# Optimization experiments

Measured on AMD Instinct MI355X. Metric: run time of the kernel, lower is better.

Reference implementation:

```python
import jax, jax.numpy as jnp
import numpy as np

MAX_DET = 300   # max_det in non_max_suppression
IMG = 640       # input image H=W
MH = MW = 160   # proto mask resolution
NM = 32         # mask coefficients
ALPHA = 0.6
MARGIN = 15


def setup_inputs() -> dict:
    key = jax.random.key(0)
    k1, k2, k3, k4, k5, k6 = jax.random.split(key, 6)
    na = 8400
    # realistic YOLOv8 raw head output: xywh in pixels, 1 class score in (0,1), 32 mask coeffs
    cxcy = jax.random.uniform(k1, (1, 2, na), minval=0.0, maxval=float(IMG))
    wh = jax.random.uniform(k2, (1, 2, na), minval=10.0, maxval=200.0)
    cls = jax.random.uniform(k3, (1, 1, na))
    mcoef = jax.random.normal(k4, (1, NM, na))
    prediction = jnp.concatenate([cxcy, wh, cls, mcoef], axis=1)  # [1,37,8400]
    proto = jax.random.normal(k5, (1, NM, MH, MW))
    img = jax.random.uniform(k6, (1, 3, IMG, IMG))
    return {"prediction": prediction, "proto": proto, "img": img,
            "conf_thres": jnp.float32(0.25), "iou_thres": jnp.float32(0.45)}


def _xywh2xyxy(x):
    cx, cy, w, h = x[..., 0], x[..., 1], x[..., 2], x[..., 3]
    return jnp.stack([cx - w / 2, cy - h / 2, cx + w / 2, cy + h / 2], axis=-1)


def _box_iou(b):  # b: [K,4] xyxy -> [K,K] pairwise IoU (torchvision convention)
    x1, y1, x2, y2 = b[:, 0], b[:, 1], b[:, 2], b[:, 3]
    area = (x2 - x1) * (y2 - y1)
    iw = jnp.clip(jnp.minimum(x2[:, None], x2[None, :]) - jnp.maximum(x1[:, None], x1[None, :]), 0)
    ih = jnp.clip(jnp.minimum(y2[:, None], y2[None, :]) - jnp.maximum(y1[:, None], y1[None, :]), 0)
    inter = iw * ih
    return inter / (area[:, None] + area[None, :] - inter + 1e-7)


def _nms_keep(iou, valid, iou_thres):
    # sequential greedy suppression over score-sorted boxes (padded, fixed K)
    K = iou.shape[0]
    def body(keep, i):
        suppressed = jnp.any(keep & (iou[i] > iou_thres))
        keep = keep.at[i].set(valid[i] & ~suppressed)
        return keep, None
    keep, _ = jax.lax.scan(body, jnp.zeros((K,), bool), jnp.arange(K))
    return keep


def reference(prediction, proto, img, conf_thres, iou_thres):
    # --- decode: [1,37,na] -> [na,37], xywh->xyxy (bs=1, nc=1, class offset c = 0*max_wh = 0)
    p = prediction[0].T                      # [na,37]
    boxes = _xywh2xyxy(p[:, :4])             # [na,4]
    conf = p[:, 4]                           # nc=1 -> max over classes is the class itself, j=0
    mcoef = p[:, 5:]                         # [na,32]
    valid = conf > conf_thres
    score = jnp.where(valid, conf, -1.0)
    order = jnp.argsort(-score)[:MAX_DET]    # top max_det candidates by confidence
    boxes_k, score_k, m_k = boxes[order], score[order], mcoef[order]
    valid_k = valid[order]
    # --- NMS (padded)
    keep = _nms_keep(_box_iou(boxes_k), valid_k, iou_thres)  # [K] bool
    # --- process_mask: linear combine protos, sigmoid, crop, bilinear upsample, >0.5
    masks = jax.nn.sigmoid(m_k @ proto[0].reshape(NM, -1)).reshape(MAX_DET, MH, MW)
    scale = jnp.array([MW / IMG, MH / IMG, MW / IMG, MH / IMG], dtype=boxes_k.dtype)
    db = boxes_k * scale                     # downsampled bboxes [K,4]
    r = jnp.arange(MW, dtype=masks.dtype)[None, None, :]
    c = jnp.arange(MH, dtype=masks.dtype)[None, :, None]
    crop = ((r >= db[:, 0, None, None]) & (r < db[:, 2, None, None]) &
            (c >= db[:, 1, None, None]) & (c < db[:, 3, None, None]))
    masks = masks * crop
    masks_up = jax.image.resize(masks, (MAX_DET, IMG, IMG), method='linear')  # align_corners=False bilinear
    masks_bin = (masks_up > 0.5) & keep[:, None, None]       # invalid/suppressed rows zeroed
    # --- scale_boxes: img1_shape == img0_shape -> gain=1, pad=0, just clip
    boxes_c = jnp.clip(boxes_k, 0.0, float(IMG))
    results = jnp.concatenate([boxes_c, score_k[:, None], jnp.zeros((MAX_DET, 1), boxes_c.dtype)], axis=1)
    results = results * keep[:, None].astype(results.dtype)  # [K,6] padded detections
    # --- max-area box -> crop window coords
    areas = jnp.where(keep, (boxes_c[:, 2] - boxes_c[:, 0]) * (boxes_c[:, 3] - boxes_c[:, 1]), 0.0)
    mb = jnp.where(jnp.any(keep), boxes_c[jnp.argmax(areas)], jnp.zeros(4, boxes_c.dtype))
    y1 = jnp.maximum(mb[1].astype(jnp.int32) - MARGIN, 0)
    y2 = jnp.minimum(mb[3].astype(jnp.int32) + MARGIN, IMG)
    x1 = jnp.maximum(mb[0].astype(jnp.int32) - MARGIN, 0)
    x2 = jnp.minimum(mb[2].astype(jnp.int32) + MARGIN, IMG)
    crop_coords = jnp.stack([y1, y2, x1, x2])
    # --- mask overlay blending (stack over images, sum over detections)
    stacked_mk = jnp.sum(masks_bin.astype(img.dtype), axis=0)[None]  # [1,640,640]
    pixels = jnp.count_nonzero(stacked_mk)
    blue = jnp.zeros((3, IMG, IMG), img.dtype).at[2].set(1.0)
    img_out = (1.0 - stacked_mk) * img + stacked_mk * (ALPHA * img + (1.0 - ALPHA) * blue)
    return results, keep, masks_bin, pixels, img_out, crop_coords
```

## Files before the change

kernel.cpp:

```cpp
#include <hip/hip_runtime.h>
#include <stdint.h>

#define NA 8400
#define MAXD 300
#define NMC 32
#define IMGD 640
#define MH 160
#define MW 160
#define PROTO_HW (MH*MW)
#define IMG_HW (IMGD*IMGD)

#define OFF_RESULTS 0
#define OFF_KEEP    1800
#define OFF_MASKS   2100
#define OFF_PIXELS  (2100 + 300*IMG_HW)
#define OFF_IMG     (OFF_PIXELS + 1)
#define OFF_CROP    (OFF_IMG + 3*IMG_HW)

#define WSO_MASKS160 0
#define WSO_META     (MAXD*PROTO_HW*4)
#define WSO_BOXES    (WSO_META + 64)
#define WSO_MCOEF    (WSO_BOXES + MAXD*16)
#define WSO_KEEPI    (WSO_MCOEF + MAXD*NMC*4)
#define WSO_KLIST    (WSO_KEEPI + MAXD*4)
#define WSO_EBOX     (WSO_KLIST + MAXD*4)

__global__ __launch_bounds__(1024)
void k_selnms(const float* __restrict__ pred, const float* __restrict__ conf_thres_p,
              const float* __restrict__ iou_thres_p,
              int* __restrict__ keepi, int* __restrict__ klist, int* __restrict__ meta,
              int* __restrict__ ebox, float* __restrict__ boxes_k,
              float* __restrict__ mcoef_k, float* __restrict__ out) {
    __shared__ unsigned cum[1024];
    __shared__ uint64_t kl[2048];
    __shared__ uint64_t srt[MAXD];
    __shared__ int s_cnt, s_bcut, s_nsel;
    __shared__ int sorder[MAXD];
    __shared__ int svf[MAXD];
    __shared__ float sscore[MAXD];
    __shared__ float bx[MAXD][4];
    __shared__ float sarea[MAXD];
    __shared__ uint64_t su[MAXD][5];
    __shared__ int skeep[MAXD];
    int t = threadIdx.x;
    float th = *conf_thres_p;

    cum[t] = 0;
    __syncthreads();
    for (int i = t; i < NA; i += 1024) {
        float conf = pred[4 * NA + i];
        if (conf > th) {
            int bin = (int)(conf * 1024.0f);
            bin = bin < 0 ? 0 : (bin > 1023 ? 1023 : bin);
            atomicAdd(&cum[bin], 1u);
        }
    }
    __syncthreads();
    for (int off = 1; off < 1024; off <<= 1) {
        unsigned v = cum[t] + ((t + off < 1024) ? cum[t + off] : 0u);
        __syncthreads();
        cum[t] = v;
        __syncthreads();
    }
    if (t == 0) {
        s_cnt = 0;
        int tot = (int)cum[0];
        s_nsel = tot < MAXD ? tot : MAXD;
        s_bcut = 0;
    }
    __syncthreads();
    int nsel = s_nsel;
    if (nsel > 0) {
        if (cum[t] >= (unsigned)nsel && (t == 1023 || cum[t + 1] < (unsigned)nsel))
            s_bcut = t;
    }
    __syncthreads();
    int bcut = s_bcut;
    if (nsel > 0) {
        for (int i = t; i < NA; i += 1024) {
            float conf = pred[4 * NA + i];
            if (conf > th) {
                int bin = (int)(conf * 1024.0f);
                bin = bin < 0 ? 0 : (bin > 1023 ? 1023 : bin);
                if (bin >= bcut) {
                    int p = atomicAdd(&s_cnt, 1);
                    if (p < 2048) {
                        unsigned fb = __float_as_uint(conf);
                        kl[p] = ((uint64_t)fb << 32) | (unsigned)(NA - 1 - i);
                    }
                }
            }
        }
    }
    __syncthreads();
    int cnt = s_cnt < 2048 ? s_cnt : 2048;
    for (int c = t; c < cnt; c += 1024) {
        uint64_t key = kl[c];
        int rank = 0;
        for (int j = 0; j < cnt; j++) rank += (kl[j] > key) ? 1 : 0;
        if (rank < MAXD) srt[rank] = key;
    }
    __syncthreads();
    if (t < MAXD) {
        int v = (t < nsel) ? 1 : 0;
        uint64_t key = v ? srt[t] : 0;
        int idx = v ? (NA - 1 - (int)(key & 0xffffffffu)) : 0;
        sorder[t] = idx; svf[t] = v;
        sscore[t] = v ? __uint_as_float((unsigned)(key >> 32)) : -1.0f;
        float cx = pred[0 * NA + idx], cy = pred[1 * NA + idx];
        float w = pred[2 * NA + idx], h = pred[3 * NA + idx];
        float b0 = cx - w * 0.5f, b1 = cy - h * 0.5f, b2 = cx + w * 0.5f, b3 = cy + h * 0.5f;
        if (!v) { b0 = b1 = b2 = b3 = 0.f; }
        bx[t][0] = b0; bx[t][1] = b1; bx[t][2] = b2; bx[t][3] = b3;
        sarea[t] = (b2 - b0) * (b3 - b1);
        boxes_k[t * 4 + 0] = b0; boxes_k[t * 4 + 1] = b1;
        boxes_k[t * 4 + 2] = b2; boxes_k[t * 4 + 3] = b3;
    }
    __syncthreads();
    for (int m = t; m < MAXD * NMC; m += 1024) {
        int r = m >> 5, c = m & 31;
        mcoef_k[m] = svf[r] ? pred[(5 + c) * NA + sorder[r]] : 0.f;
    }
    float ithr = *iou_thres_p;
    if (t < MAXD) {
        float x1 = bx[t][0], y1 = bx[t][1], x2 = bx[t][2], y2 = bx[t][3];
        float ar = sarea[t];
        uint64_t m[5] = {0, 0, 0, 0, 0};
        for (int j = 0; j < MAXD; j++) {
            float iw = fmaxf(fminf(x2, bx[j][2]) - fmaxf(x1, bx[j][0]), 0.f);
            float ih = fmaxf(fminf(y2, bx[j][3]) - fmaxf(y1, bx[j][1]), 0.f);
            float inter = iw * ih;
            float iou = inter / (ar + sarea[j] - inter + 1e-7f);
            if (iou > ithr) m[j >> 6] |= 1ull << (j & 63);
        }
        for (int w = 0; w < 5; w++) su[t][w] = m[w];
        float db0 = x1 * 0.25f, db1 = y1 * 0.25f, db2 = x2 * 0.25f, db3 = y2 * 0.25f;
        int pxmin = max(0, (int)ceilf(db0));
        int pxmax = min(MW - 1, (int)ceilf(db2) - 1);
        int pymin = max(0, (int)ceilf(db1));
        int pymax = min(MH - 1, (int)ceilf(db3) - 1);
        int xlo = 1, xhi = 0, ylo = 1, yhi = 0;
        if (pxmin <= pxmax && pymin <= pymax) {
            xlo = max(0, 4 * pxmin - 2); xhi = min(IMGD - 1, 4 * pxmax + 5);
            ylo = max(0, 4 * pymin - 2); yhi = min(IMGD - 1, 4 * pymax + 5);
        }
        ebox[t * 4 + 0] = xlo; ebox[t * 4 + 1] = xhi;
        ebox[t * 4 + 2] = ylo; ebox[t * 4 + 3] = yhi;
    }
    __syncthreads();
    if (t < 64) {
        uint64_t kwl = 0;
        int lane = t;
        for (int i = 0; i < MAXD; i++) {
            uint64_t x = (lane < 5) ? (su[i][lane] & kwl) : 0;
            bool sup = __any(x != 0);
            bool k = svf[i] && !sup;
            if (lane == (i >> 6) && k) kwl |= 1ull << (i & 63);
            if (lane == 0) { skeep[i] = k ? 1 : 0; keepi[i] = k ? 1 : 0; }
        }
    }
    __syncthreads();
    if (t < MAXD) {
        bool k = skeep[t] != 0;
        float bc0 = fminf(fmaxf(bx[t][0], 0.f), 640.f);
        float bc1 = fminf(fmaxf(bx[t][1], 0.f), 640.f);
        float bc2 = fminf(fmaxf(bx[t][2], 0.f), 640.f);
        float bc3 = fminf(fmaxf(bx[t][3], 0.f), 640.f);
        out[OFF_RESULTS + t * 6 + 0] = k ? bc0 : 0.f;
        out[OFF_RESULTS + t * 6 + 1] = k ? bc1 : 0.f;
        out[OFF_RESULTS + t * 6 + 2] = k ? bc2 : 0.f;
        out[OFF_RESULTS + t * 6 + 3] = k ? bc3 : 0.f;
        out[OFF_RESULTS + t * 6 + 4] = k ? sscore[t] : 0.f;
        out[OFF_RESULTS + t * 6 + 5] = 0.f;
        out[OFF_KEEP + t] = k ? 1.f : 0.f;
    }
    if (t == 0) {
        int n = 0;
        bool anyk = false;
        for (int i = 0; i < MAXD; i++)
            if (skeep[i]) { klist[n++] = i; anyk = true; }
        meta[0] = n;
        meta[1] = 0;
        float amax = -INFINITY; int ai = 0;
        for (int i = 0; i < MAXD; i++) {
            float bc0 = fminf(fmaxf(bx[i][0], 0.f), 640.f);
            float bc1 = fminf(fmaxf(bx[i][1], 0.f), 640.f);
            float bc2 = fminf(fmaxf(bx[i][2], 0.f), 640.f);
            float bc3 = fminf(fmaxf(bx[i][3], 0.f), 640.f);
            float a = skeep[i] ? (bc2 - bc0) * (bc3 - bc1) : 0.f;
            if (a > amax) { amax = a; ai = i; }
        }
        float mb0 = 0.f, mb1 = 0.f, mb2 = 0.f, mb3 = 0.f;
        if (anyk) {
            mb0 = fminf(fmaxf(bx[ai][0], 0.f), 640.f);
            mb1 = fminf(fmaxf(bx[ai][1], 0.f), 640.f);
            mb2 = fminf(fmaxf(bx[ai][2], 0.f), 640.f);
            mb3 = fminf(fmaxf(bx[ai][3], 0.f), 640.f);
        }
        int y1 = max((int)mb1 - 15, 0);
        int y2 = min((int)mb3 + 15, IMGD);
        int x1 = max((int)mb0 - 15, 0);
        int x2 = min((int)mb2 + 15, IMGD);
        out[OFF_CROP + 0] = (float)y1;
        out[OFF_CROP + 1] = (float)y2;
        out[OFF_CROP + 2] = (float)x1;
        out[OFF_CROP + 3] = (float)x2;
    }
}

__global__ __launch_bounds__(256)
void k_masks(const float* __restrict__ proto, const float* __restrict__ mcoef_k,
             const float* __restrict__ boxes_k, const int* __restrict__ keepi,
             float* __restrict__ masks160) {
    int slot = blockIdx.y;
    if (!keepi[slot]) return;
    __shared__ float co[NMC];
    __shared__ float db[4];
    int t = threadIdx.x;
    if (t < NMC) co[t] = mcoef_k[slot * NMC + t];
    if (t >= NMC && t < NMC + 4) db[t - NMC] = boxes_k[slot * 4 + (t - NMC)] * 0.25f;
    __syncthreads();
    int p4 = (blockIdx.x * 256 + t) * 4;
    float4 acc = {0.f, 0.f, 0.f, 0.f};
#pragma unroll
    for (int k = 0; k < NMC; k++) {
        float4 pv = *(const float4*)(proto + k * PROTO_HW + p4);
        float ck = co[k];
        acc.x = fmaf(ck, pv.x, acc.x);
        acc.y = fmaf(ck, pv.y, acc.y);
        acc.z = fmaf(ck, pv.z, acc.z);
        acc.w = fmaf(ck, pv.w, acc.w);
    }
    int py = p4 / MW, px0 = p4 - py * MW;
    float c = (float)py;
    bool rowin = (c >= db[1]) && (c < db[3]);
    float4 o;
    float r0 = (float)px0, r1 = r0 + 1.f, r2 = r0 + 2.f, r3 = r0 + 3.f;
    o.x = (rowin && r0 >= db[0] && r0 < db[2]) ? 1.f / (1.f + expf(-acc.x)) : 0.f;
    o.y = (rowin && r1 >= db[0] && r1 < db[2]) ? 1.f / (1.f + expf(-acc.y)) : 0.f;
    o.z = (rowin && r2 >= db[0] && r2 < db[2]) ? 1.f / (1.f + expf(-acc.z)) : 0.f;
    o.w = (rowin && r3 >= db[0] && r3 < db[2]) ? 1.f / (1.f + expf(-acc.w)) : 0.f;
    *(float4*)(masks160 + slot * PROTO_HW + p4) = o;
}

__device__ __forceinline__ float bilin(const float* __restrict__ m, int y, int x) {
    float sy = 0.25f * (float)y - 0.375f;
    float sx = 0.25f * (float)x - 0.375f;
    int y0 = (int)floorf(sy); float fy = sy - (float)y0;
    int x0 = (int)floorf(sx); float fx = sx - (float)x0;
    if (y0 < 0) { y0 = 0; fy = 0.f; }
    int y1 = y0 + 1; if (y1 > MH - 1) { y1 = MH - 1; fy = 0.f; }
    if (x0 < 0) { x0 = 0; fx = 0.f; }
    int x1 = x0 + 1; if (x1 > MW - 1) { x1 = MW - 1; fx = 0.f; }
    const float* r0 = m + y0 * MW;
    const float* r1 = m + y1 * MW;
    float v00 = r0[x0], v01 = r0[x1], v10 = r1[x0], v11 = r1[x1];
    float t0 = fmaf(fy, v10, (1.f - fy) * v00);
    float t1 = fmaf(fy, v11, (1.f - fy) * v01);
    return fmaf(fx, t1, (1.f - fx) * t0);
}

__global__ __launch_bounds__(256)
void k_upsample(const float* __restrict__ masks160, const int* __restrict__ keepi,
                const int* __restrict__ ebox, float* __restrict__ out_masks) {
    int det = blockIdx.y;
    int t = threadIdx.x;
    int base = (blockIdx.x * 256 + t) * 4;
    int y = base / IMGD, x = base - y * IMGD;
    float4 o = {0.f, 0.f, 0.f, 0.f};
    if (keepi[det]) {
        int xlo = ebox[det * 4 + 0], xhi = ebox[det * 4 + 1];
        int ylo = ebox[det * 4 + 2], yhi = ebox[det * 4 + 3];
        if (y >= ylo && y <= yhi && x + 3 >= xlo && x <= xhi) {
            const float* m = masks160 + (size_t)det * PROTO_HW;
            o.x = (bilin(m, y, x)     > 0.5f) ? 1.f : 0.f;
            o.y = (bilin(m, y, x + 1) > 0.5f) ? 1.f : 0.f;
            o.z = (bilin(m, y, x + 2) > 0.5f) ? 1.f : 0.f;
            o.w = (bilin(m, y, x + 3) > 0.5f) ? 1.f : 0.f;
        }
    }
    *(float4*)(out_masks + (size_t)det * IMG_HW + base) = o;
}

__global__ __launch_bounds__(256)
void k_blend(const float* __restrict__ masks160, const int* __restrict__ klist,
             const int* __restrict__ ebox, const int* __restrict__ meta,
             const float* __restrict__ img, float* __restrict__ out,
             int* __restrict__ pix_count) {
    __shared__ int sxlo[MAXD], sxhi[MAXD], sylo[MAXD], syhi[MAXD], soff[MAXD];
    int n = meta[0];
    int t = threadIdx.x;
    for (int i = t; i < n; i += 256) {
        int d = klist[i];
        sxlo[i] = ebox[d * 4 + 0]; sxhi[i] = ebox[d * 4 + 1];
        sylo[i] = ebox[d * 4 + 2]; syhi[i] = ebox[d * 4 + 3];
        soff[i] = d * PROTO_HW;
    }
    __syncthreads();
    int base = (blockIdx.x * 256 + t) * 4;
    int y = base / IMGD, x = base - y * IMGD;
    float4 s = {0.f, 0.f, 0.f, 0.f};
    for (int i = 0; i < n; i++) {
        if (y >= sylo[i] && y <= syhi[i] && x + 3 >= sxlo[i] && x <= sxhi[i]) {
            const float* m = masks160 + soff[i];
            s.x += (bilin(m, y, x)     > 0.5f) ? 1.f : 0.f;
            s.y += (bilin(m, y, x + 1) > 0.5f) ? 1.f : 0.f;
            s.z += (bilin(m, y, x + 2) > 0.5f) ? 1.f : 0.f;
            s.w += (bilin(m, y, x + 3) > 0.5f) ? 1.f : 0.f;
        }
    }
#pragma unroll
    for (int c = 0; c < 3; c++) {
        float4 iv = *(const float4*)(img + (size_t)c * IMG_HW + base);
        float bl = (c == 2) ? 1.f : 0.f;
        float4 ov;
        ov.x = (1.f - s.x) * iv.x + s.x * (0.6f * iv.x + 0.4f * bl);
        ov.y = (1.f - s.y) * iv.y + s.y * (0.6f * iv.y + 0.4f * bl);
        ov.z = (1.f - s.z) * iv.z + s.z * (0.6f * iv.z + 0.4f * bl);
        ov.w = (1.f - s.w) * iv.w + s.w * (0.6f * iv.w + 0.4f * bl);
        *(float4*)(out + OFF_IMG + (size_t)c * IMG_HW + base) = ov;
    }
    int cnt = (s.x != 0.f) + (s.y != 0.f) + (s.z != 0.f) + (s.w != 0.f);
    for (int o2 = 32; o2 > 0; o2 >>= 1) cnt += __shfl_down(cnt, o2, 64);
    if ((t & 63) == 0) atomicAdd(pix_count, cnt);
}

__global__ void k_final(const int* __restrict__ meta, float* __restrict__ out) {
    out[OFF_PIXELS] = (float)meta[1];
}

extern "C" void kernel_launch(void* const* d_in, const int* in_sizes, int n_in,
                              void* d_out, int out_size, void* d_ws, size_t ws_size,
                              hipStream_t stream) {
    const float* pred       = (const float*)d_in[0];
    const float* proto      = (const float*)d_in[1];
    const float* img        = (const float*)d_in[2];
    const float* conf_thres = (const float*)d_in[3];
    const float* iou_thres  = (const float*)d_in[4];
    float* out = (float*)d_out;
    char* ws = (char*)d_ws;

    float* masks160 = (float*)(ws + WSO_MASKS160);
    int*   meta     = (int*)(ws + WSO_META);
    float* boxes_k  = (float*)(ws + WSO_BOXES);
    float* mcoef_k  = (float*)(ws + WSO_MCOEF);
    int*   keepi    = (int*)(ws + WSO_KEEPI);
    int*   klist    = (int*)(ws + WSO_KLIST);
    int*   ebox     = (int*)(ws + WSO_EBOX);

    k_selnms<<<dim3(1), dim3(1024), 0, stream>>>(pred, conf_thres, iou_thres,
                                                 keepi, klist, meta, ebox, boxes_k, mcoef_k, out);
    k_masks<<<dim3(PROTO_HW / 1024, MAXD), dim3(256), 0, stream>>>(proto, mcoef_k, boxes_k, keepi, masks160);
    k_upsample<<<dim3(IMG_HW / 1024, MAXD), dim3(256), 0, stream>>>(masks160, keepi, ebox, out + OFF_MASKS);
    k_blend<<<dim3(IMG_HW / 1024), dim3(256), 0, stream>>>(masks160, klist, ebox, meta, img, out, meta + 1);
    k_final<<<dim3(1), dim3(1), 0, stream>>>(meta, out);
}
```

Before: 764.0 us.

## Merge mask zero-fill into mask kernel and paint only detection boxes alongside blend

Replaces the per-detection full-image upsample kernel with two pieces. A zero-fill of the 300×640×640 mask output now runs in extra blocks of the proto-mask kernel. A box-restricted paint pass, one block per kept detection, runs in extra blocks of the blend kernel. This removes one launch and skips the bilinear work and the per-pixel checks outside each detection box, while the bulk zero-write overlaps with mask computation. Correctness depends on the fill finishing before the paint, which the stream ordering between the two kernels guarantees. Each paint block now loops serially over a whole box.

```diff
diff --git a/kernel.cpp b/kernel.cpp
--- a/kernel.cpp
+++ b/kernel.cpp
@@ -24,6 +24,10 @@
 #define WSO_KEEPI    (WSO_MCOEF + MAXD*NMC*4)
 #define WSO_KLIST    (WSO_KEEPI + MAXD*4)
 #define WSO_EBOX     (WSO_KLIST + MAXD*4)
+
+#define MASKS_BLKS (PROTO_HW / 1024 * MAXD)
+#define FILL_BLKS  2048
+#define BLEND_BLKS (IMG_HW / 1024)
 
 __global__ __launch_bounds__(1024)
 void k_selnms(const float* __restrict__ pred, const float* __restrict__ conf_thres_p,
@@ -209,18 +213,29 @@
 }
 
 __global__ __launch_bounds__(256)
-void k_masks(const float* __restrict__ proto, const float* __restrict__ mcoef_k,
-             const float* __restrict__ boxes_k, const int* __restrict__ keepi,
-             float* __restrict__ masks160) {
-    int slot = blockIdx.y;
+void k_masks_fill(const float* __restrict__ proto, const float* __restrict__ mcoef_k,
+                  const float* __restrict__ boxes_k, const int* __restrict__ keepi,
+                  float* __restrict__ masks160, float* __restrict__ out_masks) {
+    int bid = blockIdx.x;
+    int t = threadIdx.x;
+    if (bid >= MASKS_BLKS) {
+        size_t tid = (size_t)(bid - MASKS_BLKS) * 256 + t;
+        const size_t stride = (size_t)FILL_BLKS * 256;
+        const size_t nf4 = (size_t)MAXD * IMG_HW / 4;
+        float4 z = {0.f, 0.f, 0.f, 0.f};
+        float4* dst = (float4*)out_masks;
+        for (size_t i = tid; i < nf4; i += stride) dst[i] = z;
+        return;
+    }
+    int slot = bid / (PROTO_HW / 1024);
+    int chunk = bid % (PROTO_HW / 1024);
     if (!keepi[slot]) return;
     __shared__ float co[NMC];
     __shared__ float db[4];
-    int t = threadIdx.x;
     if (t < NMC) co[t] = mcoef_k[slot * NMC + t];
     if (t >= NMC && t < NMC + 4) db[t - NMC] = boxes_k[slot * 4 + (t - NMC)] * 0.25f;
     __syncthreads();
-    int p4 = (blockIdx.x * 256 + t) * 4;
+    int p4 = (chunk * 256 + t) * 4;
     float4 acc = {0.f, 0.f, 0.f, 0.f};
 #pragma unroll
     for (int k = 0; k < NMC; k++) {
@@ -261,35 +276,40 @@
 }
 
 __global__ __launch_bounds__(256)
-void k_upsample(const float* __restrict__ masks160, const int* __restrict__ keepi,
-                const int* __restrict__ ebox, float* __restrict__ out_masks) {
-    int det = blockIdx.y;
+void k_blend_paint(const float* __restrict__ masks160, const int* __restrict__ keepi,
+                   const int* __restrict__ klist, const int* __restrict__ ebox,
+                   const int* __restrict__ meta, const float* __restrict__ img,
+                   float* __restrict__ out, int* __restrict__ pix_count) {
+    int bid = blockIdx.x;
     int t = threadIdx.x;
-    int base = (blockIdx.x * 256 + t) * 4;
-    int y = base / IMGD, x = base - y * IMGD;
-    float4 o = {0.f, 0.f, 0.f, 0.f};
-    if (keepi[det]) {
+
+    if (bid >= BLEND_BLKS) {
+        int det = bid - BLEND_BLKS;
+        if (!keepi[det]) return;
         int xlo = ebox[det * 4 + 0], xhi = ebox[det * 4 + 1];
         int ylo = ebox[det * 4 + 2], yhi = ebox[det * 4 + 3];
-        if (y >= ylo && y <= yhi && x + 3 >= xlo && x <= xhi) {
-            const float* m = masks160 + (size_t)det * PROTO_HW;
-            o.x = (bilin(m, y, x)     > 0.5f) ? 1.f : 0.f;
-            o.y = (bilin(m, y, x + 1) > 0.5f) ? 1.f : 0.f;
-            o.z = (bilin(m, y, x + 2) > 0.5f) ? 1.f : 0.f;
-            o.w = (bilin(m, y, x + 3) > 0.5f) ? 1.f : 0.f;
-        }
-    }
-    *(float4*)(out_masks + (size_t)det * IMG_HW + base) = o;
-}
-
-__global__ __launch_bounds__(256)
-void k_blend(const float* __restrict__ masks160, const int* __restrict__ klist,
-             const int* __restrict__ ebox, const int* __restrict__ meta,
-             const float* __restrict__ img, float* __restrict__ out,
-             int* __restrict__ pix_count) {
+        if (xlo > xhi || ylo > yhi) return;
+        int x4lo = xlo >> 2, x4hi = xhi >> 2;
+        const float* m = masks160 + (size_t)det * PROTO_HW;
+        float* od = out + OFF_MASKS + (size_t)det * IMG_HW;
+        int lane = t & 63, wv = t >> 6;
+        for (int row = ylo + wv; row <= yhi; row += 4) {
+            float* orow = od + row * IMGD;
+            for (int c4 = x4lo + lane; c4 <= x4hi; c4 += 64) {
+                int x = c4 * 4;
+                float4 o;
+                o.x = (bilin(m, row, x)     > 0.5f) ? 1.f : 0.f;
+                o.y = (bilin(m, row, x + 1) > 0.5f) ? 1.f : 0.f;
+                o.z = (bilin(m, row, x + 2) > 0.5f) ? 1.f : 0.f;
+                o.w = (bilin(m, row, x + 3) > 0.5f) ? 1.f : 0.f;
+                *(float4*)(orow + x) = o;
+            }
+        }
+        return;
+    }
+
     __shared__ int sxlo[MAXD], sxhi[MAXD], sylo[MAXD], syhi[MAXD], soff[MAXD];
     int n = meta[0];
-    int t = threadIdx.x;
     for (int i = t; i < n; i += 256) {
         int d = klist[i];
         sxlo[i] = ebox[d * 4 + 0]; sxhi[i] = ebox[d * 4 + 1];
@@ -297,7 +317,7 @@
         soff[i] = d * PROTO_HW;
     }
     __syncthreads();
-    int base = (blockIdx.x * 256 + t) * 4;
+    int base = (bid * 256 + t) * 4;
     int y = base / IMGD, x = base - y * IMGD;
     float4 s = {0.f, 0.f, 0.f, 0.f};
     for (int i = 0; i < n; i++) {
@@ -350,8 +370,9 @@
 
     k_selnms<<<dim3(1), dim3(1024), 0, stream>>>(pred, conf_thres, iou_thres,
                                                  keepi, klist, meta, ebox, boxes_k, mcoef_k, out);
-    k_masks<<<dim3(PROTO_HW / 1024, MAXD), dim3(256), 0, stream>>>(proto, mcoef_k, boxes_k, keepi, masks160);
-    k_upsample<<<dim3(IMG_HW / 1024, MAXD), dim3(256), 0, stream>>>(masks160, keepi, ebox, out + OFF_MASKS);
-    k_blend<<<dim3(IMG_HW / 1024), dim3(256), 0, stream>>>(masks160, klist, ebox, meta, img, out, meta + 1);
+    k_masks_fill<<<dim3(MASKS_BLKS + FILL_BLKS), dim3(256), 0, stream>>>(proto, mcoef_k, boxes_k,
+                                                                         keepi, masks160, out + OFF_MASKS);
+    k_blend_paint<<<dim3(BLEND_BLKS + MAXD), dim3(256), 0, stream>>>(masks160, keepi, klist, ebox,
+                                                                     meta, img, out, meta + 1);
     k_final<<<dim3(1), dim3(1), 0, stream>>>(meta, out);
 }
```

Measured after the change: 777.6 us. No clear change (+1.8%).
